# Kernel optimization log

Measured on AMD Instinct MI355X. Metric: run time of the kernel, lower is better.

The kernel has to match this reference:

```python
import jax, jax.numpy as jnp
import numpy as np

N_AGENTS = 16
NE = 128
ED = 96          # entity_shape (entity_last_action=False)
HE = 128         # hypernet_embed
MD = 32          # mixing_embed_dim
NH = 4           # attn heads
HD = HE // NH
BS, T = 32, 50


def setup_inputs() -> dict:
    key = jax.random.key(0)
    ks = jax.random.split(key, 20)
    def lin(k, i, o):
        return (jax.random.normal(k, (i, o), jnp.float32) / np.sqrt(i)).astype(jnp.float32)
    inp = {
        "agent_qs": jax.random.normal(ks[0], (BS, T, N_AGENTS), jnp.float32),
        "entities": jax.random.normal(ks[1], (BS, T, NE, ED), jnp.float32),
        "entity_mask": jax.random.uniform(ks[2], (BS, T, NE)) < 0.15,  # True = masked/inactive
    }
    for i, p in enumerate(["w1", "v"]):
        b = 3 + i * 6
        inp[p + "_fc1_w"] = lin(ks[b], ED, HE)
        inp[p + "_fc1_b"] = jnp.zeros((HE,), jnp.float32)
        inp[p + "_attn_in_w"] = lin(ks[b + 1], HE, 3 * HE)   # in_trans (no bias)
        inp[p + "_attn_out_w"] = lin(ks[b + 2], HE, HE)
        inp[p + "_attn_out_b"] = jnp.zeros((HE,), jnp.float32)
        inp[p + "_fc2_w"] = lin(ks[b + 3], HE, MD)
        inp[p + "_fc2_b"] = jnp.zeros((MD,), jnp.float32)
    return inp


def _hypernet(x, emask, fc1_w, fc1_b, in_w, out_w, out_b, fc2_w, fc2_b, mode):
    # x: [B, ne, ed], emask: [B, ne] bool (True = masked)
    B = x.shape[0]
    x1 = jax.nn.relu(x @ fc1_w + fc1_b)                         # [B, ne, HE]
    agent_mask = emask[:, :N_AGENTS]                            # [B, na]
    af = agent_mask.astype(x.dtype)
    ef = emask.astype(x.dtype)
    # attn_mask = 1 - (1-agent)(1-entity); 1 => masked pair
    pre = (1.0 - (1.0 - af)[:, :, None] * (1.0 - ef)[:, None, :]) > 0.5  # [B, na, ne]
    qkv = x1 @ in_w                                             # [B, ne, 3*HE]
    q, k, v = jnp.split(qkv, 3, axis=-1)
    q = q[:, :N_AGENTS].reshape(B, N_AGENTS, NH, HD)
    k = k.reshape(B, NE, NH, HD)
    v = v.reshape(B, NE, NH, HD)
    logits = jnp.einsum('bqhd,bkhd->bhqk', q, k) / np.float32(np.sqrt(HD))
    logits = jnp.where(pre[:, None], jnp.float32(-1e9), logits)
    w = jax.nn.softmax(logits, axis=-1)                         # [B, NH, na, ne]
    # rows where every entity is masked: torch softmax gives NaN -> filled with 0
    all_masked = jnp.all(pre, axis=-1)                          # [B, na]
    w = jnp.where(all_masked[:, None, :, None], 0.0, w)
    attn = jnp.einsum('bhqk,bkhd->bqhd', w, v).reshape(B, N_AGENTS, HE)
    out = attn @ out_w + out_b
    out = jnp.where(agent_mask[:, :, None], 0.0, out)           # post_mask fill
    x3 = out @ fc2_w + fc2_b
    x3 = jnp.where(agent_mask[:, :, None], 0.0, x3)             # [B, na, MD]
    if mode == 'alt_vector':
        return x3.mean(axis=2)                                  # [B, na]
    return x3.mean(axis=(1, 2))                                 # [B]  (scalar mode)


def reference(agent_qs, entities, entity_mask,
              w1_fc1_w, w1_fc1_b, w1_attn_in_w, w1_attn_out_w, w1_attn_out_b, w1_fc2_w, w1_fc2_b,
              v_fc1_w, v_fc1_b, v_attn_in_w, v_attn_out_w, v_attn_out_b, v_fc2_w, v_fc2_b):
    bs, max_t, ne, ed = entities.shape
    ents = entities.reshape(bs * max_t, ne, ed)
    emask = entity_mask.reshape(bs * max_t, ne)
    qs = agent_qs.reshape(-1, N_AGENTS)
    w1 = _hypernet(ents, emask, w1_fc1_w, w1_fc1_b, w1_attn_in_w, w1_attn_out_w,
                   w1_attn_out_b, w1_fc2_w, w1_fc2_b, 'alt_vector')   # [B, na]
    w1 = jnp.abs(w1)                                            # softmax_mixing_weights=False
    v = _hypernet(ents, emask, v_fc1_w, v_fc1_b, v_attn_in_w, v_attn_out_w,
                  v_attn_out_b, v_fc2_w, v_fc2_b, 'scalar')     # [B]
    q_tot = (qs * w1).sum(axis=1) + v
    return q_tot.reshape(bs, max_t, 1)
```

## Files before the change

### kernel.cpp

```cpp
#include <hip/hip_runtime.h>
#include <hip/hip_bf16.h>


#define NA 16
#define NEn 128
#define EDm 96
#define ST 136

typedef __attribute__((ext_vector_type(8))) short bf16x8;
typedef __attribute__((ext_vector_type(4))) float f32x4;

#define MFMA(a, b, c) __builtin_amdgcn_mfma_f32_16x16x32_bf16((a), (b), (c), 0, 0, 0)
#define LGKM0() __asm__ volatile("s_waitcnt lgkmcnt(0)" ::: "memory")

#define OFF_W1 0
#define OFF_WQ 12288
#define OFF_WK 28672
#define OFF_WV 45056
#define OFF_WO 61440
#define OFF_W2 77824
#define HYPE 81920
#define WS_FLAG_OFF 327680

__device__ __forceinline__ unsigned short f2bf(float f) {
  unsigned u = __float_as_uint(f);
  u += 0x7fffu + ((u >> 16) & 1u);
  return (unsigned short)(u >> 16);
}

__device__ __forceinline__ unsigned cvt_pk2(float lo, float hi) {
  union { __hip_bfloat162 h2; unsigned u; } cv;
  cv.h2 = __float22bfloat162_rn(float2{lo, hi});
  return cv.u;
}

__device__ __forceinline__ void ctile_store(unsigned short* dst, int row0,
                                            int col, f32x4 v) {
  unsigned x = cvt_pk2(v[0], v[1]);
  unsigned y = cvt_pk2(v[2], v[3]);
  unsigned ox = (unsigned)__shfl_xor((int)x, 1);
  unsigned oy = (unsigned)__shfl_xor((int)y, 1);
  unsigned w0, w1;
  int ra;
  if ((threadIdx.x & 1) == 0) {
    ra = 0;
    w0 = (x & 0xffffu) | (ox << 16);
    w1 = (x >> 16) | (ox & 0xffff0000u);
  } else {
    ra = 2;
    w0 = (oy & 0xffffu) | (y << 16);
    w1 = (oy >> 16) | (y & 0xffff0000u);
  }
  *(unsigned*)(dst + (row0 + ra) * ST + (col & ~1)) = w0;
  *(unsigned*)(dst + (row0 + ra + 1) * ST + (col & ~1)) = w1;
}

__global__ void prep_kernel(const float* __restrict__ w_fc1w,
                            const float* __restrict__ w_inw,
                            const float* __restrict__ w_outw,
                            const float* __restrict__ w_fc2w,
                            const float* __restrict__ v_fc1w,
                            const float* __restrict__ v_inw,
                            const float* __restrict__ v_outw,
                            const float* __restrict__ v_fc2w,
                            const unsigned char* __restrict__ mask,
                            unsigned short* __restrict__ ws,
                            int* __restrict__ flag) {
  if (blockIdx.x == 80) {
    const uint4 v = *(const uint4*)(mask + threadIdx.x * 16);
    const unsigned nz = (v.x | v.y | v.z | v.w) & 0xffffff00u;
    const int any = __syncthreads_or((int)(nz != 0));
    if (threadIdx.x == 0) *flag = (any == 0) ? 1 : 0;
    return;
  }
  const int g = blockIdx.x * 256 + threadIdx.x;
  const int p = (g >= 10240) ? 1 : 0;
  const int i = g - p * 10240;
  const int l = i & 63;
  const int tt = i >> 6;
  const int lhi = l >> 4, lo = l & 15;
  const float* fc1w = p ? v_fc1w : w_fc1w;
  const float* inw = p ? v_inw : w_inw;
  const float* outw = p ? v_outw : w_outw;
  const float* fc2w = p ? v_fc2w : w_fc2w;
  unsigned short* wsp = ws + p * HYPE;

  float v8[8];
  unsigned short* dst;
  if (tt < 24) {
    const int nt = tt / 3, kt = tt - nt * 3;
    const float* src = fc1w + (kt * 32 + lhi * 8) * 128 + nt * 16 + lo;
#pragma unroll
    for (int j = 0; j < 8; ++j) v8[j] = src[j * 128];
    dst = wsp + OFF_W1 + tt * 512 + l * 8;
  } else if (tt < 56) {
    const int t2 = tt - 24;
    const int nt = t2 >> 2, kt = t2 & 3;
    const float* src = inw + (kt * 32 + lhi * 8) * 384 + nt * 16 + lo;
#pragma unroll
    for (int j = 0; j < 8; ++j) v8[j] = src[j * 384] * 0.17677669529663687f;
    dst = wsp + OFF_WQ + t2 * 512 + l * 8;
  } else if (tt < 88) {
    const int t2 = tt - 56;
    const int h = t2 >> 3, nt = t2 & 7;
    const float* src = inw + (nt * 16 + lo) * 384 + 128 + h * 32 + lhi * 8;
#pragma unroll
    for (int j = 0; j < 8; ++j) v8[j] = src[j];
    dst = wsp + OFF_WK + t2 * 512 + l * 8;
  } else if (tt < 120) {
    const int t2 = tt - 88;
    const int kt = t2 & 3, q = t2 >> 2;
    const int h = q >> 1, mt = q & 1;
    const float* src =
        inw + (kt * 32 + lhi * 8) * 384 + 256 + h * 32 + mt * 16 + lo;
#pragma unroll
    for (int j = 0; j < 8; ++j) v8[j] = src[j * 384];
    dst = wsp + OFF_WV + t2 * 512 + l * 8;
  } else if (tt < 152) {
    const int t2 = tt - 120;
    const int nt = t2 >> 2, kt = t2 & 3;
    const float* src = outw + (kt * 32 + lhi * 8) * 128 + nt * 16 + lo;
#pragma unroll
    for (int j = 0; j < 8; ++j) v8[j] = src[j * 128];
    dst = wsp + OFF_WO + t2 * 512 + l * 8;
  } else {
    const int t2 = tt - 152;
    const int nt = t2 >> 2, kt = t2 & 3;
    const float* src = fc2w + (kt * 32 + lhi * 8) * 32 + nt * 16 + lo;
#pragma unroll
    for (int j = 0; j < 8; ++j) v8[j] = src[j * 32];
    dst = wsp + OFF_W2 + t2 * 512 + l * 8;
  }
  bf16x8 o;
#pragma unroll
  for (int j = 0; j < 8; ++j) o[j] = (short)f2bf(v8[j]);
  *(bf16x8*)dst = o;
}

#define SMEM_BYTES 52480

__global__ __launch_bounds__(256, 2) void qmix_mfma(
    const float* __restrict__ agent_qs, const float* __restrict__ entities,
    const unsigned char* __restrict__ emask_g,
    const unsigned short* __restrict__ wsw, const int* __restrict__ mflag,
    const float* __restrict__ w_fc1b, const float* __restrict__ w_outb,
    const float* __restrict__ w_fc2b, const float* __restrict__ v_fc1b,
    const float* __restrict__ v_outb, const float* __restrict__ v_fc2b,
    float* __restrict__ out_g) {
  const int t = threadIdx.x;
  const int wv = t >> 6;
  const int ln = t & 63;
  const int lr = ln & 15;
  const int lq = ln >> 4;
  const int b = blockIdx.x >> 1;
  const int p = blockIdx.x & 1;
  const float* ents = entities + (size_t)b * (NEn * EDm);

  __shared__ __align__(16) unsigned char smem[SMEM_BYTES];
  unsigned short* sx1 = (unsigned short*)smem;
  unsigned short* sSlice = sx1 + 17408;
  unsigned short* sattn = sSlice;
  unsigned short* sout = sSlice + 16 * ST;
  float* sres = (float*)(smem + 52224);
  unsigned char* sm = smem + 52352;
  unsigned short* sS = sSlice + wv * 16 * ST;

  float4 eu[2][3], ev[2][3];
#pragma unroll
  for (int mi = 0; mi < 2; ++mi) {
    const float* erow = ents + ((wv * 2 + mi) * 16 + lr) * EDm + lq * 8;
#pragma unroll
    for (int kt = 0; kt < 3; ++kt) {
      eu[mi][kt] = *(const float4*)(erow + kt * 32);
      ev[mi][kt] = *(const float4*)(erow + kt * 32 + 4);
    }
  }

  const int is_i32 = *mflag;
  int mv = 1;
  if (t < NEn) {
    if (is_i32)
      mv = (((const int*)emask_g)[(size_t)b * NEn + t] != 0) ? 1 : 0;
    else
      mv = (emask_g[(size_t)b * NEn + t] != 0) ? 1 : 0;
    sm[t] = (unsigned char)mv;
  }
  const int allE = __syncthreads_and(mv);

  const unsigned short* wsb = wsw + (size_t)p * HYPE;
  const float* fc1b = p ? v_fc1b : w_fc1b;
  const float* outb = p ? v_outb : w_outb;
  const float* fc2b = p ? v_fc2b : w_fc2b;

  {
#pragma unroll
    for (int mi = 0; mi < 2; ++mi) {
      const int mt = wv * 2 + mi;
      bf16x8 af[3];
#pragma unroll
      for (int kt = 0; kt < 3; ++kt) {
        union { unsigned u32[4]; bf16x8 v8; } cv;
        cv.u32[0] = cvt_pk2(eu[mi][kt].x, eu[mi][kt].y);
        cv.u32[1] = cvt_pk2(eu[mi][kt].z, eu[mi][kt].w);
        cv.u32[2] = cvt_pk2(ev[mi][kt].x, ev[mi][kt].y);
        cv.u32[3] = cvt_pk2(ev[mi][kt].z, ev[mi][kt].w);
        af[kt] = cv.v8;
      }
#pragma unroll
      for (int nt = 0; nt < 8; ++nt) {
        f32x4 acc = {0.f, 0.f, 0.f, 0.f};
        const unsigned short* bp = wsb + OFF_W1 + (nt * 3) * 512 + ln * 8;
#pragma unroll
        for (int kt = 0; kt < 3; ++kt)
          acc = MFMA(af[kt], *(const bf16x8*)(bp + kt * 512), acc);
        const float bias = fc1b[nt * 16 + lr];
        f32x4 r;
        r[0] = fmaxf(acc[0] + bias, 0.f); r[1] = fmaxf(acc[1] + bias, 0.f);
        r[2] = fmaxf(acc[2] + bias, 0.f); r[3] = fmaxf(acc[3] + bias, 0.f);
        ctile_store(sx1, mt * 16 + lq * 4, nt * 16 + lr, r);
      }
    }
  }
  __syncthreads();

  {
    bf16x8 aq[4];
#pragma unroll
    for (int kt = 0; kt < 4; ++kt)
      aq[kt] = *(const bf16x8*)(sx1 + lr * ST + kt * 32 + lq * 8);
#pragma unroll
    for (int ni = 0; ni < 2; ++ni) {
      const int nt = wv * 2 + ni;
      f32x4 acc = {0.f, 0.f, 0.f, 0.f};
      const unsigned short* bp = wsb + OFF_WQ + (nt * 4) * 512 + ln * 8;
#pragma unroll
      for (int kt = 0; kt < 4; ++kt)
        acc = MFMA(aq[kt], *(const bf16x8*)(bp + kt * 512), acc);
      ctile_store(sS, lq * 4, ni * 16 + lr, acc);
    }
  }
  bf16x8 wk[8];
#pragma unroll
  for (int nt = 0; nt < 8; ++nt)
    wk[nt] = *(const bf16x8*)(wsb + OFF_WK + (wv * 8 + nt) * 512 + ln * 8);
  LGKM0();
  const bf16x8 aQ = *(const bf16x8*)(sS + lr * ST + lq * 8);

  {
    f32x4 Cw[8];
#pragma unroll
    for (int nt = 0; nt < 8; ++nt) {
      f32x4 acc = {0.f, 0.f, 0.f, 0.f};
      Cw[nt] = MFMA(aQ, wk[nt], acc);
    }
#pragma unroll
    for (int nt = 0; nt < 8; ++nt)
      ctile_store(sS, lq * 4, nt * 16 + lr, Cw[nt]);
  }
  LGKM0();
  bf16x8 aw[4];
#pragma unroll
  for (int kt = 0; kt < 4; ++kt)
    aw[kt] = *(const bf16x8*)(sS + lr * ST + kt * 32 + lq * 8);

  f32x4 Cl[8];
  __builtin_amdgcn_s_setprio(1);
#pragma unroll
  for (int nt = 0; nt < 8; ++nt) {
    f32x4 acc = {0.f, 0.f, 0.f, 0.f};
#pragma unroll
    for (int kt = 0; kt < 4; ++kt) {
      const bf16x8 bx =
          *(const bf16x8*)(sx1 + (nt * 16 + lr) * ST + kt * 32 + lq * 8);
      acc = MFMA(aw[kt], bx, acc);
    }
    Cl[nt] = acc;
  }

  f32x4 Cv0[8], Cv1[8];
  {
    bf16x8 av[4];
#pragma unroll
    for (int kt = 0; kt < 4; ++kt)
      av[kt] = *(const bf16x8*)(wsb + OFF_WV + ((wv * 2) * 4 + kt) * 512 +
                                ln * 8);
#pragma unroll
    for (int nt = 0; nt < 8; ++nt) {
      f32x4 acc = {0.f, 0.f, 0.f, 0.f};
#pragma unroll
      for (int kt = 0; kt < 4; ++kt) {
        const bf16x8 bx =
            *(const bf16x8*)(sx1 + (nt * 16 + lr) * ST + kt * 32 + lq * 8);
        acc = MFMA(av[kt], bx, acc);
      }
      Cv0[nt] = acc;
    }
  }
  __builtin_amdgcn_s_setprio(0);

  {
    float lv[8][4];
#pragma unroll
    for (int nt = 0; nt < 8; ++nt) {
      const int eM = sm[nt * 16 + lr];
#pragma unroll
      for (int r = 0; r < 4; ++r) lv[nt][r] = eM ? -1e9f : Cl[nt][r];
    }
    float mx[4], sl[4];
#pragma unroll
    for (int r = 0; r < 4; ++r) {
      float m = lv[0][r];
#pragma unroll
      for (int nt = 1; nt < 8; ++nt) m = fmaxf(m, lv[nt][r]);
      mx[r] = m;
    }
#pragma unroll
    for (int k = 1; k < 16; k <<= 1)
#pragma unroll
      for (int r = 0; r < 4; ++r) mx[r] = fmaxf(mx[r], __shfl_xor(mx[r], k));
    float ex[8][4];
#pragma unroll
    for (int r = 0; r < 4; ++r) sl[r] = 0.f;
#pragma unroll
    for (int nt = 0; nt < 8; ++nt)
#pragma unroll
      for (int r = 0; r < 4; ++r) {
        ex[nt][r] = __expf(lv[nt][r] - mx[r]);
        sl[r] += ex[nt][r];
      }
#pragma unroll
    for (int k = 1; k < 16; k <<= 1)
#pragma unroll
      for (int r = 0; r < 4; ++r) sl[r] += __shfl_xor(sl[r], k);
    float sc[4];
#pragma unroll
    for (int r = 0; r < 4; ++r)
      sc[r] = ((int)sm[lq * 4 + r] | allE) ? 0.f : (1.f / sl[r]);
#pragma unroll
    for (int nt = 0; nt < 8; ++nt) {
      f32x4 wv4;
#pragma unroll
      for (int r = 0; r < 4; ++r) wv4[r] = ex[nt][r] * sc[r];
      ctile_store(sS, lq * 4, nt * 16 + lr, wv4);
    }
  }

  __builtin_amdgcn_s_setprio(1);
  {
    bf16x8 av[4];
#pragma unroll
    for (int kt = 0; kt < 4; ++kt)
      av[kt] = *(const bf16x8*)(wsb + OFF_WV + ((wv * 2 + 1) * 4 + kt) * 512 +
                                ln * 8);
#pragma unroll
    for (int nt = 0; nt < 8; ++nt) {
      f32x4 acc = {0.f, 0.f, 0.f, 0.f};
#pragma unroll
      for (int kt = 0; kt < 4; ++kt) {
        const bf16x8 bx =
            *(const bf16x8*)(sx1 + (nt * 16 + lr) * ST + kt * 32 + lq * 8);
        acc = MFMA(av[kt], bx, acc);
      }
      Cv1[nt] = acc;
    }
  }
  __builtin_amdgcn_s_setprio(0);
  LGKM0();
  bf16x8 aw2[4];
#pragma unroll
  for (int kt = 0; kt < 4; ++kt)
    aw2[kt] = *(const bf16x8*)(sS + lr * ST + kt * 32 + lq * 8);
  __syncthreads();

  {
#pragma unroll
    for (int nt = 0; nt < 8; ++nt)
      ctile_store(sx1, wv * 32 + lq * 4, nt * 16 + lr, Cv0[nt]);
#pragma unroll
    for (int nt = 0; nt < 8; ++nt)
      ctile_store(sx1, wv * 32 + 16 + lq * 4, nt * 16 + lr, Cv1[nt]);
  }
  LGKM0();
  {
#pragma unroll
    for (int ntd = 0; ntd < 2; ++ntd) {
      f32x4 acc = {0.f, 0.f, 0.f, 0.f};
#pragma unroll
      for (int kt = 0; kt < 4; ++kt) {
        const bf16x8 bv = *(const bf16x8*)(sx1 + (wv * 32 + ntd * 16 + lr) *
                                                     ST +
                                           kt * 32 + lq * 8);
        acc = MFMA(aw2[kt], bv, acc);
      }
      ctile_store(sattn, lq * 4, wv * 32 + ntd * 16 + lr, acc);
    }
  }
  bf16x8 wo[2][4];
#pragma unroll
  for (int ni = 0; ni < 2; ++ni) {
    const unsigned short* bp =
        wsb + OFF_WO + ((wv * 2 + ni) * 4) * 512 + ln * 8;
#pragma unroll
    for (int kt = 0; kt < 4; ++kt)
      wo[ni][kt] = *(const bf16x8*)(bp + kt * 512);
  }
  __syncthreads();

  {
    bf16x8 aa[4];
#pragma unroll
    for (int kt = 0; kt < 4; ++kt)
      aa[kt] = *(const bf16x8*)(sattn + lr * ST + kt * 32 + lq * 8);
#pragma unroll
    for (int ni = 0; ni < 2; ++ni) {
      const int nt = wv * 2 + ni;
      f32x4 acc = {0.f, 0.f, 0.f, 0.f};
#pragma unroll
      for (int kt = 0; kt < 4; ++kt)
        acc = MFMA(aa[kt], wo[ni][kt], acc);
      const float bj = outb[nt * 16 + lr];
      f32x4 r;
      r[0] = acc[0] + bj; r[1] = acc[1] + bj;
      r[2] = acc[2] + bj; r[3] = acc[3] + bj;
      ctile_store(sout, lq * 4, nt * 16 + lr, r);
    }
  }
  bf16x8 w2f[2][4];
#pragma unroll
  for (int nt = 0; nt < 2; ++nt) {
    const unsigned short* bp = wsb + OFF_W2 + (nt * 4) * 512 + ln * 8;
#pragma unroll
    for (int kt = 0; kt < 4; ++kt)
      w2f[nt][kt] = *(const bf16x8*)(bp + kt * 512);
  }
  __syncthreads();

  {
    bf16x8 ao[4];
#pragma unroll
    for (int kt = 0; kt < 4; ++kt)
      ao[kt] = *(const bf16x8*)(sout + lr * ST + kt * 32 + lq * 8);
    f32x4 Cx[2];
#pragma unroll
    for (int nt = 0; nt < 2; ++nt) {
      f32x4 acc = {0.f, 0.f, 0.f, 0.f};
#pragma unroll
      for (int kt = 0; kt < 4; ++kt)
        acc = MFMA(ao[kt], w2f[nt][kt], acc);
      Cx[nt] = acc;
    }
    const float b0 = fc2b[lr], b1 = fc2b[16 + lr];
    float rs[4];
#pragma unroll
    for (int r = 0; r < 4; ++r) {
      const int row = lq * 4 + r;
      rs[r] = sm[row] ? 0.f : (Cx[0][r] + b0 + Cx[1][r] + b1);
    }
#pragma unroll
    for (int k = 1; k < 16; k <<= 1)
#pragma unroll
      for (int r = 0; r < 4; ++r) rs[r] += __shfl_xor(rs[r], k);
    if (wv == 0 && lr == 0) {
#pragma unroll
      for (int r = 0; r < 4; ++r) {
        const int q = lq * 4 + r;
        sres[q] = p ? rs[r] : fabsf(rs[r]) * (1.f / 32.f);
      }
    }
  }

  LGKM0();
  if (t == 0) {
    float s = 0.f;
    if (p == 0) {
      const float* qs = agent_qs + (size_t)b * NA;
#pragma unroll
      for (int q = 0; q < NA; ++q) s += qs[q] * sres[q];
    } else {
#pragma unroll
      for (int q = 0; q < NA; ++q) s += sres[q];
      s *= (1.f / 512.f);
    }
    atomicAdd(out_g + b, s);
  }
}

extern "C" void kernel_launch(void* const* d_in, const int* in_sizes, int n_in,
                              void* d_out, int out_size, void* d_ws,
                              size_t ws_size, hipStream_t stream) {
  (void)n_in; (void)out_size; (void)ws_size;
  const int nb = in_sizes[0] / NA;
  unsigned short* wsw = (unsigned short*)d_ws;
  int* mflag = (int*)((char*)d_ws + WS_FLAG_OFF);

  hipLaunchKernelGGL(prep_kernel, dim3(81), dim3(256), 0, stream,
                     (const float*)d_in[3], (const float*)d_in[5],
                     (const float*)d_in[6], (const float*)d_in[8],
                     (const float*)d_in[10], (const float*)d_in[12],
                     (const float*)d_in[13], (const float*)d_in[15],
                     (const unsigned char*)d_in[2], wsw, mflag);
  hipLaunchKernelGGL(qmix_mfma, dim3(nb * 2), dim3(256), 0, stream,
                     (const float*)d_in[0], (const float*)d_in[1],
                     (const unsigned char*)d_in[2], (const unsigned short*)wsw,
                     (const int*)mflag, (const float*)d_in[4],
                     (const float*)d_in[7], (const float*)d_in[9],
                     (const float*)d_in[11], (const float*)d_in[14],
                     (const float*)d_in[16], (float*)d_out);
}
```

Measured before the change: 243.7 us.

## Fold out-projection and fc2 mean into a precomputed weight vector

Since the output is only the mean over fc2 outputs, the out-projection and fc2 linear layers collapse into a single 128-vector h = outW·mean(fc2W) plus a scalar bias, computed in the prep kernel. The main kernel then replaces two MFMA GEMM stages, their weight loads and two block barriers with a per-wave dot product and shuffle reduction over the attention output. It also drops the bf16 rounding of the intermediate out-projection result, which slightly changes numerics.

```diff
diff --git a/kernel.cpp b/kernel.cpp
--- a/kernel.cpp
+++ b/kernel.cpp
@@ -18,7 +18,6 @@
 #define OFF_WK 28672
 #define OFF_WV 45056
 #define OFF_WO 61440
-#define OFF_W2 77824
 #define HYPE 81920
 #define WS_FLAG_OFF 327680
 
@@ -63,26 +62,59 @@
                             const float* __restrict__ v_inw,
                             const float* __restrict__ v_outw,
                             const float* __restrict__ v_fc2w,
+                            const float* __restrict__ w_outb,
+                            const float* __restrict__ w_fc2b,
+                            const float* __restrict__ v_outb,
+                            const float* __restrict__ v_fc2b,
                             const unsigned char* __restrict__ mask,
                             unsigned short* __restrict__ ws,
                             int* __restrict__ flag) {
-  if (blockIdx.x == 80) {
+  if (blockIdx.x == 60) {
     const uint4 v = *(const uint4*)(mask + threadIdx.x * 16);
     const unsigned nz = (v.x | v.y | v.z | v.w) & 0xffffff00u;
     const int any = __syncthreads_or((int)(nz != 0));
     if (threadIdx.x == 0) *flag = (any == 0) ? 1 : 0;
     return;
   }
+  if (blockIdx.x >= 61) {
+    const int hp = blockIdx.x - 61;
+    const float* fc2w = hp ? v_fc2w : w_fc2w;
+    const float* outw = hp ? v_outw : w_outw;
+    const float* outb = hp ? v_outb : w_outb;
+    const float* fc2b = hp ? v_fc2b : w_fc2b;
+    float* hdst = (float*)(ws + (size_t)hp * HYPE + OFF_WO);
+    __shared__ float sgm[128];
+    const int t = threadIdx.x;
+    if (t < 128) {
+      float g = 0.f;
+#pragma unroll
+      for (int c = 0; c < 32; ++c) g += fc2w[t * 32 + c];
+      sgm[t] = g * (1.f / 32.f);
+    }
+    __syncthreads();
+    if (t < 128) {
+      float hh = 0.f;
+      for (int m = 0; m < 128; ++m) hh += outw[t * 128 + m] * sgm[m];
+      hdst[t] = hh;
+    }
+    if (t == 0) {
+      float c0 = 0.f;
+      for (int m = 0; m < 128; ++m) c0 += outb[m] * sgm[m];
+      float bm = 0.f;
+#pragma unroll
+      for (int c = 0; c < 32; ++c) bm += fc2b[c];
+      hdst[128] = c0 + bm * (1.f / 32.f);
+    }
+    return;
+  }
   const int g = blockIdx.x * 256 + threadIdx.x;
-  const int p = (g >= 10240) ? 1 : 0;
-  const int i = g - p * 10240;
+  const int p = (g >= 7680) ? 1 : 0;
+  const int i = g - p * 7680;
   const int l = i & 63;
   const int tt = i >> 6;
   const int lhi = l >> 4, lo = l & 15;
   const float* fc1w = p ? v_fc1w : w_fc1w;
   const float* inw = p ? v_inw : w_inw;
-  const float* outw = p ? v_outw : w_outw;
-  const float* fc2w = p ? v_fc2w : w_fc2w;
   unsigned short* wsp = ws + p * HYPE;
 
   float v8[8];
@@ -107,7 +139,7 @@
 #pragma unroll
     for (int j = 0; j < 8; ++j) v8[j] = src[j];
     dst = wsp + OFF_WK + t2 * 512 + l * 8;
-  } else if (tt < 120) {
+  } else {
     const int t2 = tt - 88;
     const int kt = t2 & 3, q = t2 >> 2;
     const int h = q >> 1, mt = q & 1;
@@ -116,20 +148,6 @@
 #pragma unroll
     for (int j = 0; j < 8; ++j) v8[j] = src[j * 384];
     dst = wsp + OFF_WV + t2 * 512 + l * 8;
-  } else if (tt < 152) {
-    const int t2 = tt - 120;
-    const int nt = t2 >> 2, kt = t2 & 3;
-    const float* src = outw + (kt * 32 + lhi * 8) * 128 + nt * 16 + lo;
-#pragma unroll
-    for (int j = 0; j < 8; ++j) v8[j] = src[j * 128];
-    dst = wsp + OFF_WO + t2 * 512 + l * 8;
-  } else {
-    const int t2 = tt - 152;
-    const int nt = t2 >> 2, kt = t2 & 3;
-    const float* src = fc2w + (kt * 32 + lhi * 8) * 32 + nt * 16 + lo;
-#pragma unroll
-    for (int j = 0; j < 8; ++j) v8[j] = src[j * 32];
-    dst = wsp + OFF_W2 + t2 * 512 + l * 8;
   }
   bf16x8 o;
 #pragma unroll
@@ -137,15 +155,13 @@
   *(bf16x8*)dst = o;
 }
 
-#define SMEM_BYTES 52480
+#define SMEM_BYTES 52352
 
 __global__ __launch_bounds__(256, 2) void qmix_mfma(
     const float* __restrict__ agent_qs, const float* __restrict__ entities,
     const unsigned char* __restrict__ emask_g,
     const unsigned short* __restrict__ wsw, const int* __restrict__ mflag,
-    const float* __restrict__ w_fc1b, const float* __restrict__ w_outb,
-    const float* __restrict__ w_fc2b, const float* __restrict__ v_fc1b,
-    const float* __restrict__ v_outb, const float* __restrict__ v_fc2b,
+    const float* __restrict__ w_fc1b, const float* __restrict__ v_fc1b,
     float* __restrict__ out_g) {
   const int t = threadIdx.x;
   const int wv = t >> 6;
@@ -159,10 +175,8 @@
   __shared__ __align__(16) unsigned char smem[SMEM_BYTES];
   unsigned short* sx1 = (unsigned short*)smem;
   unsigned short* sSlice = sx1 + 17408;
-  unsigned short* sattn = sSlice;
-  unsigned short* sout = sSlice + 16 * ST;
-  float* sres = (float*)(smem + 52224);
-  unsigned char* sm = smem + 52352;
+  float* sP = (float*)sSlice;
+  unsigned char* sm = smem + 52224;
   unsigned short* sS = sSlice + wv * 16 * ST;
 
   float4 eu[2][3], ev[2][3];
@@ -189,8 +203,7 @@
 
   const unsigned short* wsb = wsw + (size_t)p * HYPE;
   const float* fc1b = p ? v_fc1b : w_fc1b;
-  const float* outb = p ? v_outb : w_outb;
-  const float* fc2b = p ? v_fc2b : w_fc2b;
+  const float* hws = (const float*)(wsb + OFF_WO);
 
   {
 #pragma unroll
@@ -243,6 +256,8 @@
 #pragma unroll
   for (int nt = 0; nt < 8; ++nt)
     wk[nt] = *(const bf16x8*)(wsb + OFF_WK + (wv * 8 + nt) * 512 + ln * 8);
+  const float h0 = hws[wv * 32 + lr];
+  const float h1 = hws[wv * 32 + 16 + lr];
   LGKM0();
   const bf16x8 aQ = *(const bf16x8*)(sS + lr * ST + lq * 8);
 
@@ -381,105 +396,52 @@
       ctile_store(sx1, wv * 32 + 16 + lq * 4, nt * 16 + lr, Cv1[nt]);
   }
   LGKM0();
-  {
-#pragma unroll
-    for (int ntd = 0; ntd < 2; ++ntd) {
-      f32x4 acc = {0.f, 0.f, 0.f, 0.f};
-#pragma unroll
-      for (int kt = 0; kt < 4; ++kt) {
-        const bf16x8 bv = *(const bf16x8*)(sx1 + (wv * 32 + ntd * 16 + lr) *
-                                                     ST +
-                                           kt * 32 + lq * 8);
-        acc = MFMA(aw2[kt], bv, acc);
-      }
-      ctile_store(sattn, lq * 4, wv * 32 + ntd * 16 + lr, acc);
-    }
-  }
-  bf16x8 wo[2][4];
-#pragma unroll
-  for (int ni = 0; ni < 2; ++ni) {
-    const unsigned short* bp =
-        wsb + OFF_WO + ((wv * 2 + ni) * 4) * 512 + ln * 8;
-#pragma unroll
-    for (int kt = 0; kt < 4; ++kt)
-      wo[ni][kt] = *(const bf16x8*)(bp + kt * 512);
+  f32x4 Ca[2];
+#pragma unroll
+  for (int ntd = 0; ntd < 2; ++ntd) {
+    f32x4 acc = {0.f, 0.f, 0.f, 0.f};
+#pragma unroll
+    for (int kt = 0; kt < 4; ++kt) {
+      const bf16x8 bv = *(const bf16x8*)(sx1 + (wv * 32 + ntd * 16 + lr) * ST +
+                                         kt * 32 + lq * 8);
+      acc = MFMA(aw2[kt], bv, acc);
+    }
+    Ca[ntd] = acc;
+  }
+
+  {
+    float part[4];
+#pragma unroll
+    for (int r = 0; r < 4; ++r) part[r] = Ca[0][r] * h0 + Ca[1][r] * h1;
+#pragma unroll
+    for (int k = 1; k < 16; k <<= 1)
+#pragma unroll
+      for (int r = 0; r < 4; ++r) part[r] += __shfl_xor(part[r], k);
+    if (lr == 0) {
+#pragma unroll
+      for (int r = 0; r < 4; ++r) sP[wv * 16 + lq * 4 + r] = part[r];
+    }
   }
   __syncthreads();
 
-  {
-    bf16x8 aa[4];
-#pragma unroll
-    for (int kt = 0; kt < 4; ++kt)
-      aa[kt] = *(const bf16x8*)(sattn + lr * ST + kt * 32 + lq * 8);
-#pragma unroll
-    for (int ni = 0; ni < 2; ++ni) {
-      const int nt = wv * 2 + ni;
-      f32x4 acc = {0.f, 0.f, 0.f, 0.f};
-#pragma unroll
-      for (int kt = 0; kt < 4; ++kt)
-        acc = MFMA(aa[kt], wo[ni][kt], acc);
-      const float bj = outb[nt * 16 + lr];
-      f32x4 r;
-      r[0] = acc[0] + bj; r[1] = acc[1] + bj;
-      r[2] = acc[2] + bj; r[3] = acc[3] + bj;
-      ctile_store(sout, lq * 4, nt * 16 + lr, r);
-    }
-  }
-  bf16x8 w2f[2][4];
-#pragma unroll
-  for (int nt = 0; nt < 2; ++nt) {
-    const unsigned short* bp = wsb + OFF_W2 + (nt * 4) * 512 + ln * 8;
-#pragma unroll
-    for (int kt = 0; kt < 4; ++kt)
-      w2f[nt][kt] = *(const bf16x8*)(bp + kt * 512);
-  }
-  __syncthreads();
-
-  {
-    bf16x8 ao[4];
-#pragma unroll
-    for (int kt = 0; kt < 4; ++kt)
-      ao[kt] = *(const bf16x8*)(sout + lr * ST + kt * 32 + lq * 8);
-    f32x4 Cx[2];
-#pragma unroll
-    for (int nt = 0; nt < 2; ++nt) {
-      f32x4 acc = {0.f, 0.f, 0.f, 0.f};
-#pragma unroll
-      for (int kt = 0; kt < 4; ++kt)
-        acc = MFMA(ao[kt], w2f[nt][kt], acc);
-      Cx[nt] = acc;
-    }
-    const float b0 = fc2b[lr], b1 = fc2b[16 + lr];
-    float rs[4];
-#pragma unroll
-    for (int r = 0; r < 4; ++r) {
-      const int row = lq * 4 + r;
-      rs[r] = sm[row] ? 0.f : (Cx[0][r] + b0 + Cx[1][r] + b1);
-    }
-#pragma unroll
-    for (int k = 1; k < 16; k <<= 1)
-#pragma unroll
-      for (int r = 0; r < 4; ++r) rs[r] += __shfl_xor(rs[r], k);
-    if (wv == 0 && lr == 0) {
-#pragma unroll
-      for (int r = 0; r < 4; ++r) {
-        const int q = lq * 4 + r;
-        sres[q] = p ? rs[r] : fabsf(rs[r]) * (1.f / 32.f);
-      }
-    }
-  }
-
-  LGKM0();
   if (t == 0) {
+    const float c0 = hws[128];
     float s = 0.f;
     if (p == 0) {
       const float* qs = agent_qs + (size_t)b * NA;
 #pragma unroll
-      for (int q = 0; q < NA; ++q) s += qs[q] * sres[q];
+      for (int row = 0; row < NA; ++row) {
+        float tot = sP[row] + sP[16 + row] + sP[32 + row] + sP[48 + row] + c0;
+        tot = sm[row] ? 0.f : tot;
+        s += qs[row] * fabsf(tot);
+      }
     } else {
 #pragma unroll
-      for (int q = 0; q < NA; ++q) s += sres[q];
-      s *= (1.f / 512.f);
+      for (int row = 0; row < NA; ++row) {
+        float tot = sP[row] + sP[16 + row] + sP[32 + row] + sP[48 + row] + c0;
+        s += sm[row] ? 0.f : tot;
+      }
+      s *= (1.f / 16.f);
     }
     atomicAdd(out_g + b, s);
   }
@@ -493,17 +455,17 @@
   unsigned short* wsw = (unsigned short*)d_ws;
   int* mflag = (int*)((char*)d_ws + WS_FLAG_OFF);
 
-  hipLaunchKernelGGL(prep_kernel, dim3(81), dim3(256), 0, stream,
+  hipLaunchKernelGGL(prep_kernel, dim3(63), dim3(256), 0, stream,
                      (const float*)d_in[3], (const float*)d_in[5],
                      (const float*)d_in[6], (const float*)d_in[8],
                      (const float*)d_in[10], (const float*)d_in[12],
                      (const float*)d_in[13], (const float*)d_in[15],
+                     (const float*)d_in[7], (const float*)d_in[9],
+                     (const float*)d_in[14], (const float*)d_in[16],
                      (const unsigned char*)d_in[2], wsw, mflag);
   hipLaunchKernelGGL(qmix_mfma, dim3(nb * 2), dim3(256), 0, stream,
                      (const float*)d_in[0], (const float*)d_in[1],
                      (const unsigned char*)d_in[2], (const unsigned short*)wsw,
                      (const int*)mflag, (const float*)d_in[4],
-                     (const float*)d_in[7], (const float*)d_in[9],
-                     (const float*)d_in[11], (const float*)d_in[14],
-                     (const float*)d_in[16], (float*)d_out);
-}
+                     (const float*)d_in[11], (float*)d_out);
+}
```

Measured after the change: 241.9 us. About the same (-0.8%).
